# Optimization experiments

Measured on AMD Instinct MI355X. Metric: run time of the kernel, lower is better.

Reference implementation:

```python
import jax, jax.numpy as jnp
import numpy as np
import math

GROUPS = 16
EPS = 1e-5

def setup_inputs() -> dict:
    key = jax.random.key(0)
    ks = jax.random.split(key, 6)
    c = 256
    x = jax.random.normal(ks[0], (4, c, 64, 64), dtype=jnp.float32)
    gn_w = jnp.ones((c,), dtype=jnp.float32)
    gn_b = jnp.zeros((c,), dtype=jnp.float32)
    qkv_w = jax.random.normal(ks[1], (3 * c, c), dtype=jnp.float32) * (1.0 / math.sqrt(c))
    qkv_b = jax.random.normal(ks[2], (3 * c,), dtype=jnp.float32) * 0.02
    proj_w = jax.random.normal(ks[3], (c, c), dtype=jnp.float32) * (1.0 / math.sqrt(c))
    proj_b = jax.random.normal(ks[4], (c,), dtype=jnp.float32) * 0.02
    return {"x": x, "gn_w": gn_w, "gn_b": gn_b, "qkv_w": qkv_w,
            "qkv_b": qkv_b, "proj_w": proj_w, "proj_b": proj_b}

def group_norm(x, w, b):
    bsz, c, h, wd = x.shape
    xg = x.reshape(bsz, GROUPS, c // GROUPS, h, wd)
    mu = xg.mean(axis=(2, 3, 4), keepdims=True)
    var = xg.var(axis=(2, 3, 4), keepdims=True)
    xn = ((xg - mu) * jax.lax.rsqrt(var + EPS)).reshape(bsz, c, h, wd)
    return xn * w[None, :, None, None] + b[None, :, None, None]

def reference(x, gn_w, gn_b, qkv_w, qkv_b, proj_w, proj_b):
    b, c, h, w = x.shape
    xn = group_norm(x, gn_w, gn_b)
    # 1x1 conv == channel matmul: [b,3c,h,w]
    qkv = jnp.einsum('oc,bchw->bohw', qkv_w, xn) + qkv_b[None, :, None, None]
    q, k, v = jnp.split(qkv, 3, axis=1)          # each [b,c,h,w]
    n = h * w
    q = q.reshape(b, c, n).transpose(0, 2, 1)    # [b,n,c]
    k = k.reshape(b, c, n)                       # [b,c,n]
    v = v.reshape(b, c, n).transpose(0, 2, 1)    # [b,n,c]
    scores = jnp.einsum('bqc,bck->bqk', q, k) / jnp.sqrt(jnp.float32(c))
    attn = jax.nn.softmax(scores, axis=-1)       # [b,n,n]
    out = jnp.einsum('bqk,bkc->bqc', attn, v)    # [b,n,c]
    out = out.transpose(0, 2, 1).reshape(b, c, h, w)
    out = jnp.einsum('oc,bchw->bohw', proj_w, out) + proj_b[None, :, None, None]
    return x + out
```

## Files before the change

### kernel.cpp

```cpp
#include <hip/hip_runtime.h>


typedef unsigned short u16;
typedef unsigned char  u8;
typedef __attribute__((ext_vector_type(8)))  short short8;
typedef __attribute__((ext_vector_type(4)))  float f32x4;
typedef __attribute__((ext_vector_type(16))) float f32x16;

#define XN_OFF   0ull
#define OP_OFF   0ull
#define QW_OFF   33554432ull
#define KW_OFF   37748736ull
#define VW_OFF   41943040ull
#define LP_OFF   46137344ull
#define WQB_OFF  46399488ull
#define WPB_OFF  46792704ull

#define QSCALE 0.09016844f

__device__ __forceinline__ u16 f2bf(float x){
  unsigned u = __float_as_uint(x);
  u += 0x7fffu + ((u >> 16) & 1u);
  return (u16)(u >> 16);
}
__device__ __forceinline__ float bf2f(u16 h){
  return __uint_as_float(((unsigned)h) << 16);
}
__device__ __forceinline__ u8 f2fp8(float x){
  return (u8)(__builtin_amdgcn_cvt_pk_fp8_f32(x, x, 0, false) & 0xff);
}
__device__ __forceinline__ float fast_exp2(float x){
  float r;
  asm("v_exp_f32 %0, %1" : "=v"(r) : "v"(x));
  return r;
}

__global__ __launch_bounds__(256) void gnw_k(const float* __restrict__ x, const float* __restrict__ wq,
                                             const float* __restrict__ wp, float* __restrict__ pstats,
                                             u16* __restrict__ wqb, u16* __restrict__ wpb){
  int t = threadIdx.x;
  if (blockIdx.y < 64){
    int bg = blockIdx.y, sl = blockIdx.x;
    const float* base = x + (size_t)bg*65536 + (size_t)sl*8192;
    float s = 0.f, ss = 0.f;
    for (int i = t; i < 2048; i += 256){
      float4 v = ((const float4*)base)[i];
      s  += (v.x + v.y) + (v.z + v.w);
      ss += (v.x*v.x + v.y*v.y) + (v.z*v.z + v.w*v.w);
    }
    for (int off = 32; off; off >>= 1){ s += __shfl_down(s, off, 64); ss += __shfl_down(ss, off, 64); }
    __shared__ float red[8];
    int wave = t >> 6, lane = t & 63;
    if (lane == 0){ red[wave] = s; red[4 + wave] = ss; }
    __syncthreads();
    if (t == 0){
      pstats[(bg*8 + sl)*2]     = red[0] + red[1] + red[2] + red[3];
      pstats[(bg*8 + sl)*2 + 1] = red[4] + red[5] + red[6] + red[7];
    }
  } else {
    int chunk = (blockIdx.y - 64)*8 + blockIdx.x;
    for (int it = 0; it < 16; ++it){
      int i = chunk*4096 + it*256 + t;
      int elem = i*4;
      float4 v = (elem < 196608) ? ((const float4*)wq)[i] : ((const float4*)wp)[i - 49152];
      uint2 w;
      w.x = (unsigned)f2bf(v.x) | ((unsigned)f2bf(v.y) << 16);
      w.y = (unsigned)f2bf(v.z) | ((unsigned)f2bf(v.w) << 16);
      if (elem < 196608) *(uint2*)(wqb + elem)          = w;
      else               *(uint2*)(wpb + elem - 196608) = w;
    }
  }
}

__global__ __launch_bounds__(256) void gn_apply_k(const float* __restrict__ x, const float* __restrict__ gw,
                                                  const float* __restrict__ gb, const float* __restrict__ pstats,
                                                  u16* __restrict__ xn){
  int b = blockIdx.z, c0 = blockIdx.y*64, n0 = blockIdx.x*64;
  __shared__ float tile[64*65];
  __shared__ float gmu[4], grs[4];
  int t = threadIdx.x;
  if (t < 4){
    int gidx = (b*16 + (c0 >> 4) + t)*8;
    float S = 0.f, SS = 0.f;
    for (int k2 = 0; k2 < 8; ++k2){ S += pstats[(gidx + k2)*2]; SS += pstats[(gidx + k2)*2 + 1]; }
    float mu = S*(1.f/65536.f);
    gmu[t] = mu;
    grs[t] = rsqrtf(SS*(1.f/65536.f) - mu*mu + 1e-5f);
  }
  __syncthreads();
  for (int i = 0; i < 4; ++i){
    int idx = i*256 + t;
    int cl = idx >> 4, q4 = idx & 15;
    int c = c0 + cl;
    float4 v = *(const float4*)(x + ((size_t)b*256 + c)*4096 + n0 + q4*4);
    float mu = gmu[cl>>4], rs = grs[cl>>4];
    float w = gw[c], bi = gb[c];
    tile[cl*65 + q4*4 + 0] = (v.x - mu)*rs*w + bi;
    tile[cl*65 + q4*4 + 1] = (v.y - mu)*rs*w + bi;
    tile[cl*65 + q4*4 + 2] = (v.z - mu)*rs*w + bi;
    tile[cl*65 + q4*4 + 3] = (v.w - mu)*rs*w + bi;
  }
  __syncthreads();
  for (int i = 0; i < 4; ++i){
    int idx = i*256 + t;
    int nl = idx >> 4, cq = idx & 15;
    int cl = cq*4;
    uint2 w;
    w.x = (unsigned)f2bf(tile[(cl+0)*65 + nl]) | ((unsigned)f2bf(tile[(cl+1)*65 + nl]) << 16);
    w.y = (unsigned)f2bf(tile[(cl+2)*65 + nl]) | ((unsigned)f2bf(tile[(cl+3)*65 + nl]) << 16);
    *(uint2*)(xn + ((size_t)b*4096 + n0 + nl)*256 + c0 + cl) = w;
  }
}

#define LDA 40
#define LDB 72
__global__ __launch_bounds__(256) void qkv_gemm_k(const u16* __restrict__ xn, const u16* __restrict__ wq,
        const float* __restrict__ qb, u8* __restrict__ q, u8* __restrict__ k, u8* __restrict__ v){
  int bx = blockIdx.x;
  int m0 = blockIdx.y*128;
  int b  = blockIdx.z;
  __shared__ u16 smem[2*128*LDB];
  u16* As = smem;
  u16* Bs = smem + 128*LDB;
  int t = threadIdx.x, lane = t & 63, wave = t >> 6;
  int wm = wave >> 1, wn = wave & 1;
  int c15 = lane & 15, g = lane >> 4;
  f32x4 acc[4][4];
  for (int mt = 0; mt < 4; ++mt) for (int nt = 0; nt < 4; ++nt) acc[mt][nt] = (f32x4){0.f,0.f,0.f,0.f};
  const u16* abase = xn + ((size_t)b*4096 + m0)*256;
  const u16* bbase = wq + (size_t)bx*128*256;
  for (int kk = 0; kk < 4; ++kk){
    int k0 = kk*64;
    for (int it = 0; it < 4; ++it){
      int idx = it*256 + t;
      int row = idx >> 3, ch = idx & 7;
      uint4 va = *(const uint4*)(abase + (size_t)row*256 + k0 + ch*8);
      *(uint4*)(As + row*LDB + ch*8) = va;
      uint4 vb = *(const uint4*)(bbase + (size_t)row*256 + k0 + ch*8);
      *(uint4*)(Bs + row*LDB + ch*8) = vb;
    }
    __syncthreads();
    for (int half = 0; half < 2; ++half){
      short8 af[4], bfr[4];
      for (int mt = 0; mt < 4; ++mt) af[mt]  = *(const short8*)(As + (wm*64 + mt*16 + c15)*LDB + half*32 + g*8);
      for (int nt = 0; nt < 4; ++nt) bfr[nt] = *(const short8*)(Bs + (wn*64 + nt*16 + c15)*LDB + half*32 + g*8);
      for (int mt = 0; mt < 4; ++mt)
        for (int nt = 0; nt < 4; ++nt)
          acc[mt][nt] = __builtin_amdgcn_mfma_f32_16x16x32_bf16(af[mt], bfr[nt], acc[mt][nt], 0, 0, 0);
    }
    __syncthreads();
  }
  if (bx < 2){
    for (int nt = 0; nt < 4; ++nt){
      int col = bx*128 + wn*64 + nt*16 + c15;
      float bias = qb[col];
      for (int mt = 0; mt < 4; ++mt){
        int m = m0 + wm*64 + mt*16 + g*4;
        for (int r = 0; r < 4; ++r)
          q[((size_t)b*4096 + m + r)*256 + col] = f2fp8(acc[mt][nt][r] + bias);
      }
    }
  } else if (bx < 4){
    for (int nt = 0; nt < 4; ++nt){
      int col = bx*128 + wn*64 + nt*16 + c15;
      int c = col - 256;
      float bias = qb[col];
      for (int mt = 0; mt < 4; ++mt){
        int m = m0 + wm*64 + mt*16 + g*4;
        for (int r = 0; r < 4; ++r){
          int n = m + r;
          size_t addr = ((size_t)b*128 + (n >> 5))*8192 +
                        (size_t)((n & 31)*256 + (((c >> 3) ^ (n & 15)) << 3) + (c & 7));
          k[addr] = f2fp8(acc[mt][nt][r] + bias);
        }
      }
    }
  } else {
    __syncthreads();
    char* Tb = (char*)smem;
    for (int nt = 0; nt < 4; ++nt){
      int o_l = wn*64 + nt*16 + c15;
      float bias = qb[bx*128 + o_l];
      for (int mt = 0; mt < 4; ++mt){
        int mb = wm*64 + mt*16 + g*4;
        unsigned p0 = (unsigned)f2bf(acc[mt][nt][0] + bias) | ((unsigned)f2bf(acc[mt][nt][1] + bias) << 16);
        unsigned p1 = (unsigned)f2bf(acc[mt][nt][2] + bias) | ((unsigned)f2bf(acc[mt][nt][3] + bias) << 16);
        int base = o_l*256 + (((mb >> 3) ^ (o_l & 7)) << 4) + ((mb & 7) << 1);
        *(unsigned*)(Tb + base)     = p0;
        *(unsigned*)(Tb + base + 4) = p1;
      }
    }
    __syncthreads();
    for (int it = 0; it < 8; ++it){
      int idx = it*256 + t;
      int ro = idx >> 4, ch = idx & 15;
      uint4 val = *(const uint4*)(Tb + ro*256 + ((ch ^ (ro & 7)) << 4));
      int c = bx*128 - 512 + ro;
      int n = m0 + ch*8;
      float f0 = bf2f((u16)(val.x & 0xffff)), f1 = bf2f((u16)(val.x >> 16));
      float f2 = bf2f((u16)(val.y & 0xffff)), f3 = bf2f((u16)(val.y >> 16));
      float f4 = bf2f((u16)(val.z & 0xffff)), f5 = bf2f((u16)(val.z >> 16));
      float f6 = bf2f((u16)(val.w & 0xffff)), f7 = bf2f((u16)(val.w >> 16));
      int w0 = __builtin_amdgcn_cvt_pk_fp8_f32(f0, f1, 0, false);
      w0     = __builtin_amdgcn_cvt_pk_fp8_f32(f2, f3, w0, true);
      int w1 = __builtin_amdgcn_cvt_pk_fp8_f32(f4, f5, 0, false);
      w1     = __builtin_amdgcn_cvt_pk_fp8_f32(f6, f7, w1, true);
      size_t addr = ((size_t)b*128 + (n >> 5))*8192 +
                    (size_t)(c*32 + ((((n >> 3) & 3) ^ ((c >> 2) & 3)) << 3));
      uint2 wv; wv.x = (unsigned)w0; wv.y = (unsigned)w1;
      *(uint2*)(v + addr) = wv;
    }
  }
}

__global__ __launch_bounds__(256, 2) void flash_k(const u8* __restrict__ q, const u8* __restrict__ kt,
                                                  const u8* __restrict__ vt, u16* __restrict__ opart,
                                                  float* __restrict__ lpart){
  int n0 = blockIdx.x*128;
  int jh = blockIdx.y;
  int b  = blockIdx.z;
  __shared__ char buf[2][16384];
  int t = threadIdx.x, lane = t & 63, wave = t >> 6;
  int il = lane & 31;
  int h  = lane >> 5;

  uint2 qf[16];
  const u8* qrow = q + ((size_t)b*4096 + n0 + wave*32 + il)*256;
  #pragma unroll
  for (int s = 0; s < 16; ++s) qf[s] = *(const uint2*)(qrow + s*16 + h*8);

  f32x16 oacc[8];
  #pragma unroll
  for (int ct = 0; ct < 8; ++ct){
    #pragma unroll
    for (int r = 0; r < 16; ++r) oacc[ct][r] = 0.f;
  }
  float lsum = 0.f;

  size_t tb0 = ((size_t)b*128 + jh*32) * 8192;
  const char* gK = (const char*)kt + tb0;
  const char* gV = (const char*)vt + tb0;
  const char* gsrc = (wave < 2) ? (gK + wave*4096) : (gV + (wave - 2)*4096);
  unsigned lds_off = wave*4096;

  {
    const char* g0 = gsrc + (size_t)lane*16;
    #pragma unroll
    for (int i = 0; i < 4; ++i)
      __builtin_amdgcn_global_load_lds((const __attribute__((address_space(1))) void*)(g0 + i*1024),
          (__attribute__((address_space(3))) void*)((char*)buf[0] + lds_off + i*1024), 16, 0, 0);
    const char* g1 = gsrc + 8192 + (size_t)lane*16;
    #pragma unroll
    for (int i = 0; i < 4; ++i)
      __builtin_amdgcn_global_load_lds((const __attribute__((address_space(1))) void*)(g1 + i*1024),
          (__attribute__((address_space(3))) void*)((char*)buf[1] + lds_off + i*1024), 16, 0, 0);
  }

  for (int jt = 0; jt < 32; ++jt){
    int p = jt & 1;
    asm volatile("" ::: "memory");
    if (jt < 31) __builtin_amdgcn_s_waitcnt(0x0F74);
    else         __builtin_amdgcn_s_waitcnt(0x0F70);
    __builtin_amdgcn_s_barrier();
    asm volatile("" ::: "memory");

    const char* klds = buf[p];
    const char* vlds = buf[p] + 8192;

    f32x16 s0, s1;
    #pragma unroll
    for (int r = 0; r < 16; ++r){ s0[r] = 0.f; s1[r] = 0.f; }
    #pragma unroll
    for (int s = 0; s < 16; s += 2){
      long kf0 = *(const long*)(klds + il*256 + (((2*s + h)       ^ (il & 15)) << 3));
      long kf1 = *(const long*)(klds + il*256 + (((2*(s+1) + h)   ^ (il & 15)) << 3));
      s0 = __builtin_amdgcn_mfma_f32_32x32x16_fp8_fp8(kf0, *(const long*)&qf[s],   s0, 0, 0, 0);
      s1 = __builtin_amdgcn_mfma_f32_32x32x16_fp8_fp8(kf1, *(const long*)&qf[s+1], s1, 0, 0, 0);
    }
    float pv[16];
    #pragma unroll
    for (int r = 0; r < 16; ++r){
      float e = fast_exp2((s0[r] + s1[r]) * QSCALE);
      pv[r] = e;
      lsum += e;
    }
    long pa[2];
    #pragma unroll
    for (int s2 = 0; s2 < 2; ++s2){
      int q0 = __builtin_amdgcn_cvt_pk_fp8_f32(pv[8*s2+0], pv[8*s2+1], 0, false);
      q0     = __builtin_amdgcn_cvt_pk_fp8_f32(pv[8*s2+2], pv[8*s2+3], q0, true);
      int q1 = __builtin_amdgcn_cvt_pk_fp8_f32(pv[8*s2+4], pv[8*s2+5], 0, false);
      q1     = __builtin_amdgcn_cvt_pk_fp8_f32(pv[8*s2+6], pv[8*s2+7], q1, true);
      int e  = h ? q0 : q1;
      int rr = __shfl_xor(e, 32, 64);
      unsigned lo = (unsigned)(h ? rr : q0);
      unsigned hi = (unsigned)(h ? q1 : rr);
      pa[s2] = ((long)hi << 32) | (long)lo;
    }
    #pragma unroll
    for (int s2 = 0; s2 < 2; ++s2){
      #pragma unroll
      for (int ct = 0; ct < 8; ++ct){
        int c = ct*32 + il;
        long vf = *(const long*)(vlds + c*32 + (((2*s2 + h) ^ ((c >> 2) & 3)) << 3));
        oacc[ct] = __builtin_amdgcn_mfma_f32_32x32x16_fp8_fp8(pa[s2], vf, oacc[ct], 0, 0, 0);
      }
    }

    asm volatile("" ::: "memory");
    __builtin_amdgcn_s_waitcnt(0xC07F);
    __builtin_amdgcn_s_barrier();
    asm volatile("" ::: "memory");
    if (jt + 2 < 32){
      const char* gn2 = gsrc + (size_t)(jt + 2)*8192 + (size_t)lane*16;
      #pragma unroll
      for (int i = 0; i < 4; ++i)
        __builtin_amdgcn_global_load_lds((const __attribute__((address_space(1))) void*)(gn2 + i*1024),
            (__attribute__((address_space(3))) void*)((char*)buf[p] + lds_off + i*1024), 16, 0, 0);
    }
  }

  float tot = lsum + __shfl_xor(lsum, 32, 64);
  if (h == 0) lpart[(size_t)(jh*4 + b)*4096 + n0 + wave*32 + il] = tot;
  u16* obase = opart + ((size_t)(jh*4 + b)*4096 + n0 + wave*32)*256;
  #pragma unroll
  for (int ct = 0; ct < 8; ++ct){
    #pragma unroll
    for (int r = 0; r < 16; ++r){
      int i = (r & 3) + 8*(r >> 2) + 4*h;
      obase[(size_t)i*256 + ct*32 + il] = f2bf(oacc[ct][r]);
    }
  }
}

__global__ __launch_bounds__(256) void proj_gemm_k(const u16* __restrict__ opart, const float* __restrict__ lpart,
        const u16* __restrict__ wp, const float* __restrict__ pb, const float* __restrict__ x,
        float* __restrict__ out){
  int n0 = blockIdx.x*64;
  int b  = blockIdx.y;
  __shared__ u16 As[256*LDA];
  __shared__ u16 Bs[64*LDA];
  __shared__ float linv[64];
  int t = threadIdx.x, lane = t & 63, wave = t >> 6;
  int c15 = lane & 15, g = lane >> 4;
  if (t < 64){
    size_t row = (size_t)b*4096 + n0 + t;
    linv[t] = 1.0f / (lpart[row] + lpart[16384 + row] + lpart[32768 + row] + lpart[49152 + row]);
  }
  f32x4 acc[4][4];
  for (int mt = 0; mt < 4; ++mt) for (int nt = 0; nt < 4; ++nt) acc[mt][nt] = (f32x4){0.f,0.f,0.f,0.f};
  __syncthreads();
  for (int kk = 0; kk < 8; ++kk){
    int k0 = kk*32;
    for (int it = 0; it < 4; ++it){
      int idx = it*256 + t;
      int row = idx >> 2, ch = idx & 3;
      *(uint4*)(As + row*LDA + ch*8) = *(const uint4*)(wp + (size_t)row*256 + k0 + ch*8);
    }
    {
      int row = t >> 2, ch = t & 3;
      const u16* bptr = opart + ((size_t)b*4096 + n0 + row)*256 + k0 + ch*8;
      uint4 o0 = *(const uint4*)(bptr);
      uint4 o1 = *(const uint4*)(bptr + 4194304ull);
      uint4 o2 = *(const uint4*)(bptr + 8388608ull);
      uint4 o3 = *(const uint4*)(bptr + 12582912ull);
      float inv = linv[row];
      const unsigned* u0 = (const unsigned*)&o0;
      const unsigned* u1 = (const unsigned*)&o1;
      const unsigned* u2 = (const unsigned*)&o2;
      const unsigned* u3 = (const unsigned*)&o3;
      uint4 w;
      unsigned* wpk = (unsigned*)&w;
      for (int i = 0; i < 4; ++i){
        float lo = (bf2f((u16)(u0[i] & 0xffff)) + bf2f((u16)(u1[i] & 0xffff)) +
                    bf2f((u16)(u2[i] & 0xffff)) + bf2f((u16)(u3[i] & 0xffff))) * inv;
        float hi = (bf2f((u16)(u0[i] >> 16))    + bf2f((u16)(u1[i] >> 16)) +
                    bf2f((u16)(u2[i] >> 16))    + bf2f((u16)(u3[i] >> 16)))    * inv;
        wpk[i] = (unsigned)f2bf(lo) | ((unsigned)f2bf(hi) << 16);
      }
      *(uint4*)(Bs + row*LDA + ch*8) = w;
    }
    __syncthreads();
    short8 af[4], bfr[4];
    for (int mt = 0; mt < 4; ++mt) af[mt]  = *(const short8*)(As + (wave*64 + mt*16 + c15)*LDA + g*8);
    for (int nt = 0; nt < 4; ++nt) bfr[nt] = *(const short8*)(Bs + (nt*16 + c15)*LDA + g*8);
    for (int mt = 0; mt < 4; ++mt)
      for (int nt = 0; nt < 4; ++nt)
        acc[mt][nt] = __builtin_amdgcn_mfma_f32_16x16x32_bf16(af[mt], bfr[nt], acc[mt][nt], 0, 0, 0);
    __syncthreads();
  }
  for (int mt = 0; mt < 4; ++mt){
    for (int r = 0; r < 4; ++r){
      int o = wave*64 + mt*16 + g*4 + r;
      float bias = pb[o];
      for (int nt = 0; nt < 4; ++nt){
        int n = n0 + nt*16 + c15;
        size_t off = ((size_t)b*256 + o)*4096 + n;
        out[off] = x[off] + bias + acc[mt][nt][r];
      }
    }
  }
}

extern "C" void kernel_launch(void* const* d_in, const int* in_sizes, int n_in,
                              void* d_out, int out_size, void* d_ws, size_t ws_size,
                              hipStream_t stream){
  (void)in_sizes; (void)n_in; (void)out_size; (void)ws_size;
  const float* x     = (const float*)d_in[0];
  const float* gw    = (const float*)d_in[1];
  const float* gb    = (const float*)d_in[2];
  const float* qkvw  = (const float*)d_in[3];
  const float* qkvb  = (const float*)d_in[4];
  const float* projw = (const float*)d_in[5];
  const float* projb = (const float*)d_in[6];
  float* out = (float*)d_out;
  char* ws = (char*)d_ws;

  u16*   xn    = (u16*)(ws + XN_OFF);
  u16*   op    = (u16*)(ws + OP_OFF);
  u8*    qws   = (u8*)(ws + QW_OFF);
  float* pstat = (float*)(ws + QW_OFF);
  u8*    kws   = (u8*)(ws + KW_OFF);
  u8*    vws   = (u8*)(ws + VW_OFF);
  float* lp    = (float*)(ws + LP_OFF);
  u16*   wqb   = (u16*)(ws + WQB_OFF);
  u16*   wpb   = (u16*)(ws + WPB_OFF);

  gnw_k<<<dim3(8, 66), 256, 0, stream>>>(x, qkvw, projw, pstat, wqb, wpb);
  gn_apply_k<<<dim3(64, 4, 4), 256, 0, stream>>>(x, gw, gb, pstat, xn);
  qkv_gemm_k<<<dim3(6, 32, 4), 256, 0, stream>>>(xn, wqb, qkvb, qws, kws, vws);
  flash_k<<<dim3(32, 4, 4), 256, 0, stream>>>(qws, kws, vws, op, lp);
  proj_gemm_k<<<dim3(64, 4), 256, 0, stream>>>(op, lp, wpb, projb, x, out);
}
```

Before: 170.8 us.

## Double flash K/V tile to 64 keys and vectorize QKV epilogue stores

The flash attention kernel now loads 64-key K/V tiles (32KB per buffer) instead of 32-key tiles, halving the number of barrier/prefetch iterations. The K and V workspace layouts and their swizzles are changed to match, and the QKV GEMM swaps MFMA operand order for the Q/K tiles so each lane holds four consecutive channels. That lets it write packed 4-byte fp8 stores instead of single bytes. The larger LDS footprint (64KB per block) may limit occupancy, and the per-group statistics are moved to a separate workspace offset.

```diff
diff --git a/kernel.cpp b/kernel.cpp
--- a/kernel.cpp
+++ b/kernel.cpp
@@ -7,7 +7,6 @@
 typedef __attribute__((ext_vector_type(4)))  float f32x4;
 typedef __attribute__((ext_vector_type(16))) float f32x16;
 
-#define XN_OFF   0ull
 #define OP_OFF   0ull
 #define QW_OFF   33554432ull
 #define KW_OFF   37748736ull
@@ -15,8 +14,11 @@
 #define LP_OFF   46137344ull
 #define WQB_OFF  46399488ull
 #define WPB_OFF  46792704ull
+#define ST_OFF   46923776ull
 
 #define QSCALE 0.09016844f
+#define LDA 40
+#define LDB 72
 
 __device__ __forceinline__ u16 f2bf(float x){
   unsigned u = __float_as_uint(x);
@@ -25,9 +27,6 @@
 }
 __device__ __forceinline__ float bf2f(u16 h){
   return __uint_as_float(((unsigned)h) << 16);
-}
-__device__ __forceinline__ u8 f2fp8(float x){
-  return (u8)(__builtin_amdgcn_cvt_pk_fp8_f32(x, x, 0, false) & 0xff);
 }
 __device__ __forceinline__ float fast_exp2(float x){
   float r;
@@ -112,8 +111,6 @@
   }
 }
 
-#define LDA 40
-#define LDB 72
 __global__ __launch_bounds__(256) void qkv_gemm_k(const u16* __restrict__ xn, const u16* __restrict__ wq,
         const float* __restrict__ qb, u8* __restrict__ q, u8* __restrict__ k, u8* __restrict__ v){
   int bx = blockIdx.x;
@@ -126,7 +123,7 @@
   int wm = wave >> 1, wn = wave & 1;
   int c15 = lane & 15, g = lane >> 4;
   f32x4 acc[4][4];
-  for (int mt = 0; mt < 4; ++mt) for (int nt = 0; nt < 4; ++nt) acc[mt][nt] = (f32x4){0.f,0.f,0.f,0.f};
+  for (int i = 0; i < 4; ++i) for (int j = 0; j < 4; ++j) acc[i][j] = (f32x4){0.f,0.f,0.f,0.f};
   const u16* abase = xn + ((size_t)b*4096 + m0)*256;
   const u16* bbase = wq + (size_t)bx*128*256;
   for (int kk = 0; kk < 4; ++kk){
@@ -142,37 +139,44 @@
     __syncthreads();
     for (int half = 0; half < 2; ++half){
       short8 af[4], bfr[4];
-      for (int mt = 0; mt < 4; ++mt) af[mt]  = *(const short8*)(As + (wm*64 + mt*16 + c15)*LDB + half*32 + g*8);
-      for (int nt = 0; nt < 4; ++nt) bfr[nt] = *(const short8*)(Bs + (wn*64 + nt*16 + c15)*LDB + half*32 + g*8);
-      for (int mt = 0; mt < 4; ++mt)
-        for (int nt = 0; nt < 4; ++nt)
-          acc[mt][nt] = __builtin_amdgcn_mfma_f32_16x16x32_bf16(af[mt], bfr[nt], acc[mt][nt], 0, 0, 0);
+      for (int pt = 0; pt < 4; ++pt) af[pt]  = *(const short8*)(As + (wm*64 + pt*16 + c15)*LDB + half*32 + g*8);
+      for (int ot = 0; ot < 4; ++ot) bfr[ot] = *(const short8*)(Bs + (wn*64 + ot*16 + c15)*LDB + half*32 + g*8);
+      if (bx < 4){
+        for (int ot = 0; ot < 4; ++ot)
+          for (int pt = 0; pt < 4; ++pt)
+            acc[ot][pt] = __builtin_amdgcn_mfma_f32_16x16x32_bf16(bfr[ot], af[pt], acc[ot][pt], 0, 0, 0);
+      } else {
+        for (int mt = 0; mt < 4; ++mt)
+          for (int nt = 0; nt < 4; ++nt)
+            acc[mt][nt] = __builtin_amdgcn_mfma_f32_16x16x32_bf16(af[mt], bfr[nt], acc[mt][nt], 0, 0, 0);
+      }
     }
     __syncthreads();
   }
   if (bx < 2){
-    for (int nt = 0; nt < 4; ++nt){
-      int col = bx*128 + wn*64 + nt*16 + c15;
-      float bias = qb[col];
-      for (int mt = 0; mt < 4; ++mt){
-        int m = m0 + wm*64 + mt*16 + g*4;
-        for (int r = 0; r < 4; ++r)
-          q[((size_t)b*4096 + m + r)*256 + col] = f2fp8(acc[mt][nt][r] + bias);
+    for (int ot = 0; ot < 4; ++ot){
+      int col = bx*128 + wn*64 + ot*16 + g*4;
+      float4 b4 = *(const float4*)(qb + col);
+      for (int pt = 0; pt < 4; ++pt){
+        int n = m0 + wm*64 + pt*16 + c15;
+        f32x4 a = acc[ot][pt];
+        int w0 = __builtin_amdgcn_cvt_pk_fp8_f32(a[0] + b4.x, a[1] + b4.y, 0, false);
+        w0     = __builtin_amdgcn_cvt_pk_fp8_f32(a[2] + b4.z, a[3] + b4.w, w0, true);
+        *(unsigned*)(q + ((size_t)b*4096 + n)*256 + col) = (unsigned)w0;
       }
     }
   } else if (bx < 4){
-    for (int nt = 0; nt < 4; ++nt){
-      int col = bx*128 + wn*64 + nt*16 + c15;
-      int c = col - 256;
-      float bias = qb[col];
-      for (int mt = 0; mt < 4; ++mt){
-        int m = m0 + wm*64 + mt*16 + g*4;
-        for (int r = 0; r < 4; ++r){
-          int n = m + r;
-          size_t addr = ((size_t)b*128 + (n >> 5))*8192 +
-                        (size_t)((n & 31)*256 + (((c >> 3) ^ (n & 15)) << 3) + (c & 7));
-          k[addr] = f2fp8(acc[mt][nt][r] + bias);
-        }
+    for (int ot = 0; ot < 4; ++ot){
+      int cb = (bx - 2)*128 + wn*64 + ot*16 + g*4;
+      float4 b4 = *(const float4*)(qb + 256 + cb);
+      for (int pt = 0; pt < 4; ++pt){
+        int n = m0 + wm*64 + pt*16 + c15;
+        f32x4 a = acc[ot][pt];
+        int w0 = __builtin_amdgcn_cvt_pk_fp8_f32(a[0] + b4.x, a[1] + b4.y, 0, false);
+        w0     = __builtin_amdgcn_cvt_pk_fp8_f32(a[2] + b4.z, a[3] + b4.w, w0, true);
+        size_t addr = ((size_t)b*64 + (n >> 6))*16384 +
+                      (size_t)((n & 63)*256 + (((cb >> 3) ^ (n & 15)) << 3) + (cb & 7));
+        *(unsigned*)(k + addr) = (unsigned)w0;
       }
     }
   } else {
@@ -205,8 +209,8 @@
       w0     = __builtin_amdgcn_cvt_pk_fp8_f32(f2, f3, w0, true);
       int w1 = __builtin_amdgcn_cvt_pk_fp8_f32(f4, f5, 0, false);
       w1     = __builtin_amdgcn_cvt_pk_fp8_f32(f6, f7, w1, true);
-      size_t addr = ((size_t)b*128 + (n >> 5))*8192 +
-                    (size_t)(c*32 + ((((n >> 3) & 3) ^ ((c >> 2) & 3)) << 3));
+      size_t addr = ((size_t)b*64 + (n >> 6))*16384 +
+                    (size_t)(c*64 + ((((n >> 3) & 7) ^ ((c >> 1) & 7)) << 3));
       uint2 wv; wv.x = (unsigned)w0; wv.y = (unsigned)w1;
       *(uint2*)(v + addr) = wv;
     }
@@ -219,7 +223,7 @@
   int n0 = blockIdx.x*128;
   int jh = blockIdx.y;
   int b  = blockIdx.z;
-  __shared__ char buf[2][16384];
+  __shared__ char buf[2][32768];
   int t = threadIdx.x, lane = t & 63, wave = t >> 6;
   int il = lane & 31;
   int h  = lane >> 5;
@@ -237,73 +241,77 @@
   }
   float lsum = 0.f;
 
-  size_t tb0 = ((size_t)b*128 + jh*32) * 8192;
+  size_t tb0 = ((size_t)b*64 + jh*16) * 16384;
   const char* gK = (const char*)kt + tb0;
   const char* gV = (const char*)vt + tb0;
-  const char* gsrc = (wave < 2) ? (gK + wave*4096) : (gV + (wave - 2)*4096);
-  unsigned lds_off = wave*4096;
+  const char* gsrc = (wave < 2) ? (gK + wave*8192) : (gV + (wave - 2)*8192);
+  unsigned lds_off = wave*8192;
 
   {
     const char* g0 = gsrc + (size_t)lane*16;
     #pragma unroll
-    for (int i = 0; i < 4; ++i)
+    for (int i = 0; i < 8; ++i)
       __builtin_amdgcn_global_load_lds((const __attribute__((address_space(1))) void*)(g0 + i*1024),
           (__attribute__((address_space(3))) void*)((char*)buf[0] + lds_off + i*1024), 16, 0, 0);
-    const char* g1 = gsrc + 8192 + (size_t)lane*16;
+    const char* g1 = gsrc + 16384 + (size_t)lane*16;
     #pragma unroll
-    for (int i = 0; i < 4; ++i)
+    for (int i = 0; i < 8; ++i)
       __builtin_amdgcn_global_load_lds((const __attribute__((address_space(1))) void*)(g1 + i*1024),
           (__attribute__((address_space(3))) void*)((char*)buf[1] + lds_off + i*1024), 16, 0, 0);
   }
 
-  for (int jt = 0; jt < 32; ++jt){
+  for (int jt = 0; jt < 16; ++jt){
     int p = jt & 1;
     asm volatile("" ::: "memory");
-    if (jt < 31) __builtin_amdgcn_s_waitcnt(0x0F74);
+    if (jt < 15) __builtin_amdgcn_s_waitcnt(0x0F78);
     else         __builtin_amdgcn_s_waitcnt(0x0F70);
     __builtin_amdgcn_s_barrier();
     asm volatile("" ::: "memory");
 
     const char* klds = buf[p];
-    const char* vlds = buf[p] + 8192;
-
-    f32x16 s0, s1;
+    const char* vlds = buf[p] + 16384;
+
     #pragma unroll
-    for (int r = 0; r < 16; ++r){ s0[r] = 0.f; s1[r] = 0.f; }
-    #pragma unroll
-    for (int s = 0; s < 16; s += 2){
-      long kf0 = *(const long*)(klds + il*256 + (((2*s + h)       ^ (il & 15)) << 3));
-      long kf1 = *(const long*)(klds + il*256 + (((2*(s+1) + h)   ^ (il & 15)) << 3));
-      s0 = __builtin_amdgcn_mfma_f32_32x32x16_fp8_fp8(kf0, *(const long*)&qf[s],   s0, 0, 0, 0);
-      s1 = __builtin_amdgcn_mfma_f32_32x32x16_fp8_fp8(kf1, *(const long*)&qf[s+1], s1, 0, 0, 0);
-    }
-    float pv[16];
-    #pragma unroll
-    for (int r = 0; r < 16; ++r){
-      float e = fast_exp2((s0[r] + s1[r]) * QSCALE);
-      pv[r] = e;
-      lsum += e;
-    }
-    long pa[2];
-    #pragma unroll
-    for (int s2 = 0; s2 < 2; ++s2){
-      int q0 = __builtin_amdgcn_cvt_pk_fp8_f32(pv[8*s2+0], pv[8*s2+1], 0, false);
-      q0     = __builtin_amdgcn_cvt_pk_fp8_f32(pv[8*s2+2], pv[8*s2+3], q0, true);
-      int q1 = __builtin_amdgcn_cvt_pk_fp8_f32(pv[8*s2+4], pv[8*s2+5], 0, false);
-      q1     = __builtin_amdgcn_cvt_pk_fp8_f32(pv[8*s2+6], pv[8*s2+7], q1, true);
-      int e  = h ? q0 : q1;
-      int rr = __shfl_xor(e, 32, 64);
-      unsigned lo = (unsigned)(h ? rr : q0);
-      unsigned hi = (unsigned)(h ? q1 : rr);
-      pa[s2] = ((long)hi << 32) | (long)lo;
-    }
-    #pragma unroll
-    for (int s2 = 0; s2 < 2; ++s2){
-      #pragma unroll
-      for (int ct = 0; ct < 8; ++ct){
-        int c = ct*32 + il;
-        long vf = *(const long*)(vlds + c*32 + (((2*s2 + h) ^ ((c >> 2) & 3)) << 3));
-        oacc[ct] = __builtin_amdgcn_mfma_f32_32x32x16_fp8_fp8(pa[s2], vf, oacc[ct], 0, 0, 0);
+    for (int jg = 0; jg < 2; ++jg){
+      f32x16 sA, sB;
+      #pragma unroll
+      for (int r = 0; r < 16; ++r){ sA[r] = 0.f; sB[r] = 0.f; }
+      const char* krow = klds + (jg*32 + il)*256;
+      #pragma unroll
+      for (int s = 0; s < 16; s += 2){
+        long kf0 = *(const long*)(krow + (((2*s + h)     ^ (il & 15)) << 3));
+        long kf1 = *(const long*)(krow + (((2*(s+1) + h) ^ (il & 15)) << 3));
+        sA = __builtin_amdgcn_mfma_f32_32x32x16_fp8_fp8(kf0, *(const long*)&qf[s],   sA, 0, 0, 0);
+        sB = __builtin_amdgcn_mfma_f32_32x32x16_fp8_fp8(kf1, *(const long*)&qf[s+1], sB, 0, 0, 0);
+      }
+      float pv[16];
+      #pragma unroll
+      for (int r = 0; r < 16; ++r){
+        float e = fast_exp2((sA[r] + sB[r]) * QSCALE);
+        pv[r] = e;
+        lsum += e;
+      }
+      long pa[2];
+      #pragma unroll
+      for (int s2 = 0; s2 < 2; ++s2){
+        int q0 = __builtin_amdgcn_cvt_pk_fp8_f32(pv[8*s2+0], pv[8*s2+1], 0, false);
+        q0     = __builtin_amdgcn_cvt_pk_fp8_f32(pv[8*s2+2], pv[8*s2+3], q0, true);
+        int q1 = __builtin_amdgcn_cvt_pk_fp8_f32(pv[8*s2+4], pv[8*s2+5], 0, false);
+        q1     = __builtin_amdgcn_cvt_pk_fp8_f32(pv[8*s2+6], pv[8*s2+7], q1, true);
+        int e  = h ? q0 : q1;
+        int rr = __shfl_xor(e, 32, 64);
+        unsigned lo = (unsigned)(h ? rr : q0);
+        unsigned hi = (unsigned)(h ? q1 : rr);
+        pa[s2] = ((long)hi << 32) | (long)lo;
+      }
+      #pragma unroll
+      for (int s2 = 0; s2 < 2; ++s2){
+        #pragma unroll
+        for (int ct = 0; ct < 8; ++ct){
+          int c = ct*32 + il;
+          long vf = *(const long*)(vlds + c*64 + (((jg*4 + 2*s2 + h) ^ ((c >> 1) & 7)) << 3));
+          oacc[ct] = __builtin_amdgcn_mfma_f32_32x32x16_fp8_fp8(pa[s2], vf, oacc[ct], 0, 0, 0);
+        }
       }
     }
 
@@ -311,10 +319,10 @@
     __builtin_amdgcn_s_waitcnt(0xC07F);
     __builtin_amdgcn_s_barrier();
     asm volatile("" ::: "memory");
-    if (jt + 2 < 32){
-      const char* gn2 = gsrc + (size_t)(jt + 2)*8192 + (size_t)lane*16;
-      #pragma unroll
-      for (int i = 0; i < 4; ++i)
+    if (jt + 2 < 16){
+      const char* gn2 = gsrc + (size_t)(jt + 2)*16384 + (size_t)lane*16;
+      #pragma unroll
+      for (int i = 0; i < 8; ++i)
         __builtin_amdgcn_global_load_lds((const __attribute__((address_space(1))) void*)(gn2 + i*1024),
             (__attribute__((address_space(3))) void*)((char*)buf[p] + lds_off + i*1024), 16, 0, 0);
     }
@@ -416,15 +424,16 @@
   float* out = (float*)d_out;
   char* ws = (char*)d_ws;
 
-  u16*   xn    = (u16*)(ws + XN_OFF);
   u16*   op    = (u16*)(ws + OP_OFF);
   u8*    qws   = (u8*)(ws + QW_OFF);
-  float* pstat = (float*)(ws + QW_OFF);
   u8*    kws   = (u8*)(ws + KW_OFF);
   u8*    vws   = (u8*)(ws + VW_OFF);
   float* lp    = (float*)(ws + LP_OFF);
   u16*   wqb   = (u16*)(ws + WQB_OFF);
   u16*   wpb   = (u16*)(ws + WPB_OFF);
+  float* pstat = (float*)(ws + ST_OFF);
+  u16*   xn    = (u16*)(ws + QW_OFF);
+  xn = (u16*)(ws + OP_OFF);
 
   gnw_k<<<dim3(8, 66), 256, 0, stream>>>(x, qkvw, projw, pstat, wqb, wpb);
   gn_apply_k<<<dim3(64, 4, 4), 256, 0, stream>>>(x, gw, gb, pstat, xn);
```

Result: slower. 221.1 us (+29.5%).
